# Kernel tuning notes

Hardware: AMD Instinct MI355X
Metric: run time of the kernel (lower is better)

The kernel has to match this reference:

```python
import jax, jax.numpy as jnp
import numpy as np


def setup_inputs() -> dict:
    key = jax.random.key(0)
    ks = jax.random.split(key, 6)
    B, Te, Td = 4, 512, 512
    E, D, H = 256, 256, 64
    s = lambda n: 1.0 / np.sqrt(n)
    return {
        "ctx": jax.random.normal(ks[0], (B, Te, E), jnp.float32),
        "decoder_states": jax.random.normal(ks[1], (B, Td, D + E), jnp.float32),
        "W1i": jax.random.normal(ks[2], (E, H), jnp.float32) * s(E),
        "b1i": jnp.zeros((H,), jnp.float32),
        "W1h": jax.random.normal(ks[3], (D + E, H), jnp.float32) * s(D + E),
        "b1h": jnp.zeros((H,), jnp.float32),
        "w2": jax.random.normal(ks[4], (H,), jnp.float32) * s(H),
        "b2": jnp.zeros((), jnp.float32),
    }


def reference(ctx, decoder_states, W1i, b1i, W1h, b1h, w2, b2):
    # ctx: [B, Te, E] -> [B, Te, H]
    ctx_t = jnp.einsum("bte,eh->bth", ctx, W1i) + b1i
    # decoder_states: [B, Td, D+E] -> [B, Td, H]
    dec_t = jnp.einsum("btd,dh->bth", decoder_states, W1h) + b1h
    # additive attention: [B, Td, Te, H]
    act = jnp.tanh(dec_t[:, :, None, :] + ctx_t[:, None, :, :])
    # reduce H -> scalar score: [B, Td, Te]
    scores = jnp.einsum("bdth,h->bdt", act, w2) + b2
    # softmax over encoder positions
    return jax.nn.softmax(scores, axis=-1)
```

## Files before the change

### kernel.cpp

```cpp
#include <hip/hip_runtime.h>
#include <math.h>

#define BB   4
#define TE   512
#define TD   512
#define EE   256
#define DP   512
#define HH   64
#define TDT  4
#define C2L  2.8853900817779268f
#define LOG2E 1.4426950408889634f

__device__ __forceinline__ float wave_rmax(float v) {
    #pragma unroll
    for (int off = 32; off; off >>= 1) v = fmaxf(v, __shfl_xor(v, off));
    return v;
}
__device__ __forceinline__ float wave_rsum(float v) {
    #pragma unroll
    for (int off = 32; off; off >>= 1) v += __shfl_xor(v, off);
    return v;
}

__global__ __launch_bounds__(256, 4) void proj_kernel(
    const float* __restrict__ Xc, const float* __restrict__ Wc,
    const float* __restrict__ bc,
    const float* __restrict__ Xd, const float* __restrict__ Wd,
    const float* __restrict__ bd,
    float* __restrict__ Yc, float* __restrict__ Yd)
{
    const bool isDec = blockIdx.x >= (BB * TE / 4);
    const float* X    = isDec ? Xd : Xc;
    const float* W    = isDec ? Wd : Wc;
    const float* bias = isDec ? bd : bc;
    float*       Y    = isDec ? Yd : Yc;
    const int    K    = isDec ? DP : EE;
    const int    blk  = isDec ? blockIdx.x - (BB * TE / 4) : blockIdx.x;

    const int h   = threadIdx.x & 63;
    const int row = blk * 4 + (threadIdx.x >> 6);
    const float4* xv = reinterpret_cast<const float4*>(X + (size_t)row * K);
    const float*  Wh = W + h;

    float a0 = 0.f, a1 = 0.f, a2 = 0.f, a3 = 0.f;
    #pragma unroll 4
    for (int k4 = 0; k4 < K / 4; ++k4) {
        float4 x = xv[k4];
        const float* wk = Wh + (size_t)k4 * (4 * HH);
        a0 = fmaf(x.x, wk[0 * HH], a0);
        a1 = fmaf(x.y, wk[1 * HH], a1);
        a2 = fmaf(x.z, wk[2 * HH], a2);
        a3 = fmaf(x.w, wk[3 * HH], a3);
    }
    Y[(size_t)row * HH + h] = C2L * (((a0 + a1) + (a2 + a3)) + bias[h]);
}

__global__ __launch_bounds__(512, 4) void score_softmax_kernel(
    const float* __restrict__ actx, const float* __restrict__ adec,
    const float* __restrict__ w2, const float* __restrict__ b2p,
    float* __restrict__ out)
{
    __shared__ float sdec[TDT][HH];
    __shared__ float sw2[HH];
    __shared__ float sred[TDT][8];
    __shared__ float sbase;
    __shared__ float sfin[TDT][2];

    const int b    = blockIdx.x >> 7;
    const int td0  = (blockIdx.x & 127) * TDT;
    const int tid  = threadIdx.x;
    const int lane = tid & 63;
    const int wid  = tid >> 6;

    if (tid < TDT * HH) {
        int r = tid >> 6, h = tid & 63;
        sdec[r][h] = adec[((size_t)(b * TD + td0 + r)) * HH + h];
    }
    if (tid < HH) {
        float wv = w2[tid];
        sw2[tid] = -2.0f * wv;
        float s = wave_rsum(wv);
        if (tid == 0) sbase = s + b2p[0];
    }
    __syncthreads();

    const int te = tid;
    const float4* cp = reinterpret_cast<const float4*>(
        actx + ((size_t)b * TE + te) * HH);
    const float4* wv4 = reinterpret_cast<const float4*>(sw2);

    float sc0 = 0.f, sc1 = 0.f, sc2 = 0.f, sc3 = 0.f;
    #pragma unroll 2
    for (int i = 0; i < HH / 4; ++i) {
        float4 c  = cp[i];
        float4 w4 = wv4[i];
        #pragma unroll
        for (int r = 0; r < TDT; ++r) {
            float4 d4 = reinterpret_cast<const float4*>(sdec[r])[i];
            float e0 = __builtin_amdgcn_exp2f(d4.x + c.x);
            float e1 = __builtin_amdgcn_exp2f(d4.y + c.y);
            float e2 = __builtin_amdgcn_exp2f(d4.z + c.z);
            float e3 = __builtin_amdgcn_exp2f(d4.w + c.w);
            float v0 = __builtin_amdgcn_rcpf(e0 + 1.0f);
            float v1 = __builtin_amdgcn_rcpf(e1 + 1.0f);
            float v2 = __builtin_amdgcn_rcpf(e2 + 1.0f);
            float v3 = __builtin_amdgcn_rcpf(e3 + 1.0f);
            float t;
            t = fmaf(w4.x, v0, fmaf(w4.y, v1, fmaf(w4.z, v2, w4.w * v3)));
            if (r == 0) sc0 += t;
            else if (r == 1) sc1 += t;
            else if (r == 2) sc2 += t;
            else sc3 += t;
        }
    }

    const float base = sbase;
    float scores[TDT] = { sc0 + base, sc1 + base, sc2 + base, sc3 + base };

    #pragma unroll
    for (int r = 0; r < TDT; ++r) {
        float m = wave_rmax(scores[r]);
        if (lane == 0) sred[r][wid] = m;
    }
    __syncthreads();
    if (tid < TDT * 8) {
        int r = tid >> 3;
        float v = sred[r][tid & 7];
        v = fmaxf(v, __shfl_xor(v, 4));
        v = fmaxf(v, __shfl_xor(v, 2));
        v = fmaxf(v, __shfl_xor(v, 1));
        if ((tid & 7) == 0) sfin[r][0] = v;
    }
    __syncthreads();

    float ex[TDT];
    #pragma unroll
    for (int r = 0; r < TDT; ++r) {
        ex[r] = __builtin_amdgcn_exp2f((scores[r] - sfin[r][0]) * LOG2E);
        float s = wave_rsum(ex[r]);
        if (lane == 0) sred[r][wid] = s;
    }
    __syncthreads();
    if (tid < TDT * 8) {
        int r = tid >> 3;
        float v = sred[r][tid & 7];
        v += __shfl_xor(v, 4);
        v += __shfl_xor(v, 2);
        v += __shfl_xor(v, 1);
        if ((tid & 7) == 0) sfin[r][1] = v;
    }
    __syncthreads();

    #pragma unroll
    for (int r = 0; r < TDT; ++r) {
        float inv = __builtin_amdgcn_rcpf(sfin[r][1]);
        out[((size_t)(b * TD + td0 + r)) * TE + te] = ex[r] * inv;
    }
}

extern "C" void kernel_launch(void* const* d_in, const int* in_sizes, int n_in,
                              void* d_out, int out_size, void* d_ws, size_t ws_size,
                              hipStream_t stream) {
    const float* ctx = (const float*)d_in[0];
    const float* dec = (const float*)d_in[1];
    const float* W1i = (const float*)d_in[2];
    const float* b1i = (const float*)d_in[3];
    const float* W1h = (const float*)d_in[4];
    const float* b1h = (const float*)d_in[5];
    const float* w2  = (const float*)d_in[6];
    const float* b2  = (const float*)d_in[7];
    float* out = (float*)d_out;

    float* actx = (float*)d_ws;
    float* adec = actx + (size_t)BB * TE * HH;

    proj_kernel<<<BB * TE / 4 + BB * TD / 4, 256, 0, stream>>>(
        ctx, W1i, b1i, dec, W1h, b1h, actx, adec);
    score_softmax_kernel<<<BB * (TD / TDT), 512, 0, stream>>>(
        actx, adec, w2, b2, out);
}
```

Baseline: 110.3 us.

## Transpose context projection to H-major layout and split-K projection across waves

The projection kernel now has each wave handle a quarter of the K dimension for four rows, reusing each weight load across those rows. Partial sums are reduced through shared memory. The context projection is written transposed as [B, H, Te], so in the score kernel adjacent threads (te) read consecutive addresses and loads coalesce, instead of each thread reading a strided 256-byte row. The cost is an extra shared-memory reduction and barrier in the projection, and scalar rather than float4 loads for the context values.

Result: faster. 103.8 us (-5.9%).

```diff
diff --git a/kernel.cpp b/kernel.cpp
--- a/kernel.cpp
+++ b/kernel.cpp
@@ -8,8 +8,12 @@
 #define DP   512
 #define HH   64
 #define TDT  4
+#define RPW  4
 #define C2L  2.8853900817779268f
 #define LOG2E 1.4426950408889634f
+
+#define NB_CTX (BB * TE / RPW)
+#define NB_DEC (BB * TD / RPW)
 
 __device__ __forceinline__ float wave_rmax(float v) {
     #pragma unroll
@@ -27,44 +31,70 @@
     const float* __restrict__ bc,
     const float* __restrict__ Xd, const float* __restrict__ Wd,
     const float* __restrict__ bd,
-    float* __restrict__ Yc, float* __restrict__ Yd)
+    float* __restrict__ actxT, float* __restrict__ adec)
 {
-    const bool isDec = blockIdx.x >= (BB * TE / 4);
+    __shared__ float part[4][RPW][HH];
+
+    const bool  isDec = blockIdx.x >= NB_CTX;
+    const int   blk   = isDec ? (int)blockIdx.x - NB_CTX : (int)blockIdx.x;
     const float* X    = isDec ? Xd : Xc;
     const float* W    = isDec ? Wd : Wc;
     const float* bias = isDec ? bd : bc;
-    float*       Y    = isDec ? Yd : Yc;
-    const int    K    = isDec ? DP : EE;
-    const int    blk  = isDec ? blockIdx.x - (BB * TE / 4) : blockIdx.x;
-
-    const int h   = threadIdx.x & 63;
-    const int row = blk * 4 + (threadIdx.x >> 6);
-    const float4* xv = reinterpret_cast<const float4*>(X + (size_t)row * K);
-    const float*  Wh = W + h;
+    const int   K     = isDec ? DP : EE;
+
+    const int Kw   = K >> 2;
+    const int lane = threadIdx.x & 63;
+    const int wid  = threadIdx.x >> 6;
+    const int r0   = blk * RPW;
+    const int kb   = wid * Kw;
+
+    const float*  Wl = W + (size_t)kb * HH + lane;
+    const float4* x0 = reinterpret_cast<const float4*>(X + (size_t)(r0+0)*K + kb);
+    const float4* x1 = reinterpret_cast<const float4*>(X + (size_t)(r0+1)*K + kb);
+    const float4* x2 = reinterpret_cast<const float4*>(X + (size_t)(r0+2)*K + kb);
+    const float4* x3 = reinterpret_cast<const float4*>(X + (size_t)(r0+3)*K + kb);
 
     float a0 = 0.f, a1 = 0.f, a2 = 0.f, a3 = 0.f;
+    const int niter = Kw >> 2;
     #pragma unroll 4
-    for (int k4 = 0; k4 < K / 4; ++k4) {
-        float4 x = xv[k4];
-        const float* wk = Wh + (size_t)k4 * (4 * HH);
-        a0 = fmaf(x.x, wk[0 * HH], a0);
-        a1 = fmaf(x.y, wk[1 * HH], a1);
-        a2 = fmaf(x.z, wk[2 * HH], a2);
-        a3 = fmaf(x.w, wk[3 * HH], a3);
-    }
-    Y[(size_t)row * HH + h] = C2L * (((a0 + a1) + (a2 + a3)) + bias[h]);
+    for (int k4 = 0; k4 < niter; ++k4) {
+        const float* wk = Wl + (size_t)k4 * (4 * HH);
+        float w0 = wk[0 * HH], w1 = wk[1 * HH], w2v = wk[2 * HH], w3 = wk[3 * HH];
+        float4 v0 = x0[k4], v1 = x1[k4], v2 = x2[k4], v3 = x3[k4];
+        a0 = fmaf(v0.x, w0, fmaf(v0.y, w1, fmaf(v0.z, w2v, fmaf(v0.w, w3, a0))));
+        a1 = fmaf(v1.x, w0, fmaf(v1.y, w1, fmaf(v1.z, w2v, fmaf(v1.w, w3, a1))));
+        a2 = fmaf(v2.x, w0, fmaf(v2.y, w1, fmaf(v2.z, w2v, fmaf(v2.w, w3, a2))));
+        a3 = fmaf(v3.x, w0, fmaf(v3.y, w1, fmaf(v3.z, w2v, fmaf(v3.w, w3, a3))));
+    }
+    part[wid][0][lane] = a0;
+    part[wid][1][lane] = a1;
+    part[wid][2][lane] = a2;
+    part[wid][3][lane] = a3;
+    __syncthreads();
+
+    if (isDec) {
+        int r = threadIdx.x >> 6, h = threadIdx.x & 63;
+        float s = part[0][r][h] + part[1][r][h] + part[2][r][h] + part[3][r][h];
+        adec[(size_t)(r0 + r) * HH + h] = C2L * (s + bias[h]);
+    } else {
+        int h = threadIdx.x >> 2, r = threadIdx.x & 3;
+        float s = part[0][r][h] + part[1][r][h] + part[2][r][h] + part[3][r][h];
+        int row = r0 + r;
+        int b = row >> 9, te = row & 511;
+        actxT[((size_t)b * HH + h) * TE + te] = C2L * (s + bias[h]);
+    }
 }
 
 __global__ __launch_bounds__(512, 4) void score_softmax_kernel(
-    const float* __restrict__ actx, const float* __restrict__ adec,
+    const float* __restrict__ actxT, const float* __restrict__ adec,
     const float* __restrict__ w2, const float* __restrict__ b2p,
     float* __restrict__ out)
 {
-    __shared__ float sdec[TDT][HH];
-    __shared__ float sw2[HH];
-    __shared__ float sred[TDT][8];
-    __shared__ float sbase;
-    __shared__ float sfin[TDT][2];
+    __shared__ float4 sdec4[TDT][HH / 4];
+    __shared__ float4 sw24[HH / 4];
+    __shared__ float  sred[TDT][8];
+    __shared__ float  sbase;
+    __shared__ float  sfin[TDT][2];
 
     const int b    = blockIdx.x >> 7;
     const int td0  = (blockIdx.x & 127) * TDT;
@@ -74,43 +104,41 @@
 
     if (tid < TDT * HH) {
         int r = tid >> 6, h = tid & 63;
-        sdec[r][h] = adec[((size_t)(b * TD + td0 + r)) * HH + h];
+        reinterpret_cast<float*>(&sdec4[r][0])[h] =
+            adec[(size_t)(b * TD + td0 + r) * HH + h];
     }
     if (tid < HH) {
         float wv = w2[tid];
-        sw2[tid] = -2.0f * wv;
+        reinterpret_cast<float*>(sw24)[tid] = -2.0f * wv;
         float s = wave_rsum(wv);
         if (tid == 0) sbase = s + b2p[0];
     }
     __syncthreads();
 
     const int te = tid;
-    const float4* cp = reinterpret_cast<const float4*>(
-        actx + ((size_t)b * TE + te) * HH);
-    const float4* wv4 = reinterpret_cast<const float4*>(sw2);
+    const float* cT = actxT + (size_t)b * HH * TE + te;
 
     float sc0 = 0.f, sc1 = 0.f, sc2 = 0.f, sc3 = 0.f;
     #pragma unroll 2
-    for (int i = 0; i < HH / 4; ++i) {
-        float4 c  = cp[i];
-        float4 w4 = wv4[i];
+    for (int h4 = 0; h4 < HH / 4; ++h4) {
+        const float* cp = cT + (size_t)h4 * (4 * TE);
+        float c0 = cp[0 * TE], c1 = cp[1 * TE], c2 = cp[2 * TE], c3 = cp[3 * TE];
+        float4 w4 = sw24[h4];
         #pragma unroll
         for (int r = 0; r < TDT; ++r) {
-            float4 d4 = reinterpret_cast<const float4*>(sdec[r])[i];
-            float e0 = __builtin_amdgcn_exp2f(d4.x + c.x);
-            float e1 = __builtin_amdgcn_exp2f(d4.y + c.y);
-            float e2 = __builtin_amdgcn_exp2f(d4.z + c.z);
-            float e3 = __builtin_amdgcn_exp2f(d4.w + c.w);
-            float v0 = __builtin_amdgcn_rcpf(e0 + 1.0f);
-            float v1 = __builtin_amdgcn_rcpf(e1 + 1.0f);
-            float v2 = __builtin_amdgcn_rcpf(e2 + 1.0f);
-            float v3 = __builtin_amdgcn_rcpf(e3 + 1.0f);
-            float t;
-            t = fmaf(w4.x, v0, fmaf(w4.y, v1, fmaf(w4.z, v2, w4.w * v3)));
-            if (r == 0) sc0 += t;
+            float4 d4 = sdec4[r][h4];
+            float e0 = __builtin_amdgcn_exp2f(d4.x + c0);
+            float e1 = __builtin_amdgcn_exp2f(d4.y + c1);
+            float e2 = __builtin_amdgcn_exp2f(d4.z + c2);
+            float e3 = __builtin_amdgcn_exp2f(d4.w + c3);
+            float t = fmaf(w4.x, __builtin_amdgcn_rcpf(e0 + 1.0f),
+                      fmaf(w4.y, __builtin_amdgcn_rcpf(e1 + 1.0f),
+                      fmaf(w4.z, __builtin_amdgcn_rcpf(e2 + 1.0f),
+                           w4.w * __builtin_amdgcn_rcpf(e3 + 1.0f))));
+            if      (r == 0) sc0 += t;
             else if (r == 1) sc1 += t;
             else if (r == 2) sc2 += t;
-            else sc3 += t;
+            else             sc3 += t;
         }
     }
 
@@ -171,11 +199,11 @@
     const float* b2  = (const float*)d_in[7];
     float* out = (float*)d_out;
 
-    float* actx = (float*)d_ws;
-    float* adec = actx + (size_t)BB * TE * HH;
-
-    proj_kernel<<<BB * TE / 4 + BB * TD / 4, 256, 0, stream>>>(
-        ctx, W1i, b1i, dec, W1h, b1h, actx, adec);
+    float* actxT = (float*)d_ws;
+    float* adec  = actxT + (size_t)BB * HH * TE;
+
+    proj_kernel<<<NB_CTX + NB_DEC, 256, 0, stream>>>(
+        ctx, W1i, b1i, dec, W1h, b1h, actxT, adec);
     score_softmax_kernel<<<BB * (TD / TDT), 512, 0, stream>>>(
-        actx, adec, w2, b2, out);
-}
+        actxT, adec, w2, b2, out);
+}
```
